# Performance work log

Hardware: AMD Instinct MI355X
Metric: run time of the kernel (lower is better)

The kernel has to match this reference:

```python
import jax, jax.numpy as jnp
import numpy as np

R = 0.2                 # ball-query radius (Descriptor.r)
MAX_NBRS = 64           # CONFIG['Descriptor']['max_num_neighbors']


def setup_inputs() -> dict:
    key = jax.random.key(0)
    k1, k2, k3, k4, k5, k6 = jax.random.split(key, 6)
    N, F, M = 100000, 64, 2048
    x = jax.random.normal(k1, (N, F), dtype=jnp.float32)
    pos = jax.random.normal(k2, (N, 3), dtype=jnp.float32)
    batch = jnp.sort(jax.random.randint(k3, (N,), 0, 4, dtype=jnp.int64))
    key_idx = jax.random.randint(k4, (M,), 0, N, dtype=jnp.int64)
    # MLP params: Linear(F+3 -> 128), ReLU, Linear(128 -> 128)
    H = 128
    W1 = jax.random.normal(k5, (F + 3, H), dtype=jnp.float32) / np.sqrt(F + 3)
    b1 = jnp.zeros((H,), dtype=jnp.float32)
    W2 = jax.random.normal(k6, (H, H), dtype=jnp.float32) / np.sqrt(H)
    b2 = jnp.zeros((H,), dtype=jnp.float32)
    return {"x": x, "pos": pos, "W1": W1, "b1": b1, "W2": W2, "b2": b2,
            "batch": batch, "key_idx": key_idx}


def reference(x, pos, W1, b1, W2, b2, batch, key_idx):
    N = pos.shape[0]
    qpos = pos[key_idx]            # [M,3]
    qbatch = batch[key_idx]        # [M]

    # Brute-force ball query (what torch-cluster radius does under the hood):
    # squared distances via ||q||^2 + ||p||^2 - 2 q.p  -> [M,N]
    d2 = (jnp.sum(qpos * qpos, -1)[:, None]
          + jnp.sum(pos * pos, -1)[None, :]
          - 2.0 * qpos @ pos.T)
    valid = (d2 <= R * R) & (qbatch[:, None] == batch[None, :])   # [M,N]

    # Take the first MAX_NBRS valid neighbors per query (index order, as PyG).
    order_key = jnp.where(valid, jnp.arange(N)[None, :], N)       # invalid -> N
    neg_vals, idx = jax.lax.top_k(-order_key, MAX_NBRS)           # [M,K]
    valid_k = neg_vals > -N                                       # [M,K] real edge mask

    # PointNetConv message: nn(concat([x_j, pos_j - pos_i])), then max-aggregate.
    x_j = x[idx]                                  # [M,K,F] gather
    rel = pos[idx] - qpos[:, None, :]             # [M,K,3]
    h = jnp.concatenate([x_j, rel], axis=-1)      # [M,K,F+3]
    h = jax.nn.relu(h @ W1 + b1)
    h = h @ W2 + b2                               # [M,K,H]
    h = jnp.where(valid_k[..., None], h, -jnp.inf)
    out = jnp.max(h, axis=1)                      # [M,H] max-scatter
    out = jnp.where(jnp.any(valid_k, axis=1)[:, None], out, 0.0)

    # F.normalize(out, dim=-1)
    out = out / jnp.maximum(jnp.linalg.norm(out, axis=-1, keepdims=True), 1e-12)
    return out
```

## Files before the change

### kernel.cpp

```cpp
#include <hip/hip_runtime.h>
#include <math.h>

#define MAXK 64
#define HDIM 128
#define FDIM 64

typedef __attribute__((ext_vector_type(8))) short bf16x8;
typedef __attribute__((ext_vector_type(4))) float f32x4;

__device__ __forceinline__ unsigned short f2bf(float f) {
    unsigned x = __float_as_uint(f);
    unsigned r = (x + 0x7fffu + ((x >> 16) & 1u)) >> 16;
    return (unsigned short)r;
}

__global__ __launch_bounds__(256) void prep_kernel(
    const float* __restrict__ W1, const float* __restrict__ W2,
    unsigned short* __restrict__ W1bf, unsigned short* __restrict__ W2bf)
{
    int t = blockIdx.x * 256 + threadIdx.x;
    if (t < 1536) {
        int s = t;
        int cb = s / 192, rem = s % 192, ks = rem / 64, lane = rem % 64;
        int col = cb*16 + (lane & 15);
        int k0  = ks*32 + (lane >> 4)*8;
        unsigned short v[8];
        #pragma unroll
        for (int j = 0; j < 8; ++j) {
            int k = k0 + j;
            v[j] = (k < 67) ? f2bf(W1[k*HDIM + col]) : (unsigned short)0;
        }
        uint4 p;
        p.x = (unsigned)v[0] | ((unsigned)v[1] << 16);
        p.y = (unsigned)v[2] | ((unsigned)v[3] << 16);
        p.z = (unsigned)v[4] | ((unsigned)v[5] << 16);
        p.w = (unsigned)v[6] | ((unsigned)v[7] << 16);
        *reinterpret_cast<uint4*>(&W1bf[(size_t)s*8]) = p;
    } else if (t < 1536 + 2048) {
        int s = t - 1536;
        int cb = s >> 8, ks = (s >> 6) & 3, lane = s & 63;
        int col = cb*16 + (lane & 15);
        int k0  = ks*32 + (lane >> 4)*8;
        unsigned short v[8];
        #pragma unroll
        for (int j = 0; j < 8; ++j) v[j] = f2bf(W2[(k0+j)*HDIM + col]);
        uint4 p;
        p.x = (unsigned)v[0] | ((unsigned)v[1] << 16);
        p.y = (unsigned)v[2] | ((unsigned)v[3] << 16);
        p.z = (unsigned)v[4] | ((unsigned)v[5] << 16);
        p.w = (unsigned)v[6] | ((unsigned)v[7] << 16);
        *reinterpret_cast<uint4*>(&W2bf[(size_t)s*8]) = p;
    }
}

__global__ __launch_bounds__(64) void scan_kernel(
    const float* __restrict__ pos, const int* __restrict__ batch,
    const int* __restrict__ key_idx, int N,
    int* __restrict__ lists, int* __restrict__ lcnt)
{
    int b = blockIdx.x;
    int m = b >> 2, w = b & 3;
    int lane = threadIdx.x;

    int qi = key_idx[m];
    int qb = batch[qi];
    float qx = pos[3*qi+0], qy = pos[3*qi+1], qz = pos[3*qi+2];

    int lo, hi;
    { int a=0, e=N;  while (a<e){ int mid=(a+e)>>1; if (batch[mid] <  qb) a=mid+1; else e=mid; } lo=a; }
    { int a=lo, e=N; while (a<e){ int mid=(a+e)>>1; if (batch[mid] <= qb) a=mid+1; else e=mid; } hi=a; }

    const float R2 = 0.04f;
    float q2 = __fadd_rn(__fadd_rn(__fmul_rn(qx,qx), __fmul_rn(qy,qy)), __fmul_rn(qz,qz));

    int seg   = hi - lo;
    int qlen  = (seg + 3) >> 2;
    int start = lo + w*qlen;
    int qend  = min(start + qlen, hi);

    int lc = 0;
    for (int base = start; base < qend && lc < MAXK; base += 256) {
        unsigned long long mk[4]; bool vv[4]; int jj[4];
        #pragma unroll
        for (int sub = 0; sub < 4; ++sub) {
            int j = base + sub*64 + lane;
            bool v = false;
            if (j < qend) {
                float px = pos[3*j+0], py = pos[3*j+1], pz = pos[3*j+2];
                float p2 = __fadd_rn(__fadd_rn(__fmul_rn(px,px), __fmul_rn(py,py)), __fmul_rn(pz,pz));
                float dt = __fadd_rn(__fadd_rn(__fmul_rn(qx,px), __fmul_rn(qy,py)), __fmul_rn(qz,pz));
                float d2 = __fsub_rn(__fadd_rn(q2, p2), __fmul_rn(2.0f, dt));
                v = (d2 <= R2);
            }
            mk[sub] = __ballot(v); vv[sub] = v; jj[sub] = j;
        }
        #pragma unroll
        for (int sub = 0; sub < 4; ++sub) {
            if (vv[sub]) {
                int slot = lc + (int)__popcll(mk[sub] & ((1ull << lane) - 1ull));
                if (slot < MAXK) lists[b*MAXK + slot] = jj[sub];
            }
            lc += (int)__popcll(mk[sub]);
        }
    }
    if (lane == 0) lcnt[b] = min(lc, MAXK);
}

__global__ __launch_bounds__(256) void mlp_kernel(
    const float* __restrict__ x, const float* __restrict__ pos,
    const unsigned short* __restrict__ W1bf, const unsigned short* __restrict__ W2bf,
    const float* __restrict__ b1, const float* __restrict__ b2,
    const int* __restrict__ key_idx,
    const int* __restrict__ lists, const int* __restrict__ lcnt,
    float* __restrict__ out, int M)
{
    __shared__ __align__(16) unsigned short a_lds[4*3*64*8];
    __shared__ __align__(16) unsigned short h_lds[4*16*128];
    __shared__ int   nidx[MAXK];
    __shared__ float pmax_s[4][HDIM];
    __shared__ float rsum[2];

    int m   = blockIdx.x;
    int tid = threadIdx.x;
    int lane = tid & 63, w = tid >> 6;
    int colq = lane & 15, rq = lane >> 4;

    int qi = key_idx[m];
    float qx = pos[3*qi+0], qy = pos[3*qi+1], qz = pos[3*qi+2];

    int c0 = lcnt[m*4+0], c1 = lcnt[m*4+1], c2 = lcnt[m*4+2], c3 = lcnt[m*4+3];
    int cnt = min(MAXK, c0 + c1 + c2 + c3);
    if (tid < cnt) {
        int k = tid, q, off;
        if      (k < c0)       { q = 0; off = k; }
        else if (k < c0+c1)    { q = 1; off = k - c0; }
        else if (k < c0+c1+c2) { q = 2; off = k - c0 - c1; }
        else                   { q = 3; off = k - c0 - c1 - c2; }
        nidx[tid] = lists[(m*4+q)*MAXK + off];
    }
    __syncthreads();

    #pragma unroll
    for (int i = 0; i < 3; ++i) {
        int s = tid + i*256;
        int rb = s / 192, rem = s % 192, ks = rem / 64, ln = rem % 64;
        int row = rb*16 + (ln & 15);
        int k0  = ks*32 + (ln >> 4)*8;
        unsigned short v[8];
        #pragma unroll
        for (int j = 0; j < 8; ++j) v[j] = 0;
        if (row < cnt) {
            int idx = nidx[row];
            if (ks < 2) {
                const float4* xp = reinterpret_cast<const float4*>(x + (size_t)idx*FDIM + k0);
                float4 v0 = xp[0], v1 = xp[1];
                v[0]=f2bf(v0.x); v[1]=f2bf(v0.y); v[2]=f2bf(v0.z); v[3]=f2bf(v0.w);
                v[4]=f2bf(v1.x); v[5]=f2bf(v1.y); v[6]=f2bf(v1.z); v[7]=f2bf(v1.w);
            } else if ((ln >> 4) == 0) {
                v[0] = f2bf(pos[3*idx+0] - qx);
                v[1] = f2bf(pos[3*idx+1] - qy);
                v[2] = f2bf(pos[3*idx+2] - qz);
            }
        }
        uint4 p;
        p.x = (unsigned)v[0] | ((unsigned)v[1] << 16);
        p.y = (unsigned)v[2] | ((unsigned)v[3] << 16);
        p.z = (unsigned)v[4] | ((unsigned)v[5] << 16);
        p.w = (unsigned)v[6] | ((unsigned)v[7] << 16);
        *reinterpret_cast<uint4*>(&a_lds[(size_t)s*8]) = p;
    }
    __syncthreads();

    const bf16x8* W1f = reinterpret_cast<const bf16x8*>(W1bf);
    const bf16x8* W2f = reinterpret_cast<const bf16x8*>(W2bf);

    bf16x8 a0 = *reinterpret_cast<const bf16x8*>(&a_lds[((w*3+0)*64 + lane)*8]);
    bf16x8 a1 = *reinterpret_cast<const bf16x8*>(&a_lds[((w*3+1)*64 + lane)*8]);
    bf16x8 a2 = *reinterpret_cast<const bf16x8*>(&a_lds[((w*3+2)*64 + lane)*8]);
    #pragma unroll
    for (int cb = 0; cb < 8; ++cb) {
        f32x4 c = {0.f, 0.f, 0.f, 0.f};
        c = __builtin_amdgcn_mfma_f32_16x16x32_bf16(a0, W1f[(cb*3+0)*64 + lane], c, 0, 0, 0);
        c = __builtin_amdgcn_mfma_f32_16x16x32_bf16(a1, W1f[(cb*3+1)*64 + lane], c, 0, 0, 0);
        c = __builtin_amdgcn_mfma_f32_16x16x32_bf16(a2, W1f[(cb*3+2)*64 + lane], c, 0, 0, 0);
        int col = cb*16 + colq;
        float bias = b1[col];
        #pragma unroll
        for (int reg = 0; reg < 4; ++reg) {
            int r = rq*4 + reg;
            float h = fmaxf(c[reg] + bias, 0.f);
            h_lds[w*2048 + r*128 + (col ^ ((r & 7) << 3))] = f2bf(h);
        }
    }

    int r = colq, swz = (r & 7) << 3;
    bf16x8 g0 = *reinterpret_cast<const bf16x8*>(&h_lds[w*2048 + r*128 + ((  0 + rq*8) ^ swz)]);
    bf16x8 g1 = *reinterpret_cast<const bf16x8*>(&h_lds[w*2048 + r*128 + (( 32 + rq*8) ^ swz)]);
    bf16x8 g2 = *reinterpret_cast<const bf16x8*>(&h_lds[w*2048 + r*128 + (( 64 + rq*8) ^ swz)]);
    bf16x8 g3 = *reinterpret_cast<const bf16x8*>(&h_lds[w*2048 + r*128 + (( 96 + rq*8) ^ swz)]);
    #pragma unroll
    for (int cb = 0; cb < 8; ++cb) {
        f32x4 c = {0.f, 0.f, 0.f, 0.f};
        c = __builtin_amdgcn_mfma_f32_16x16x32_bf16(g0, W2f[(cb*4+0)*64 + lane], c, 0, 0, 0);
        c = __builtin_amdgcn_mfma_f32_16x16x32_bf16(g1, W2f[(cb*4+1)*64 + lane], c, 0, 0, 0);
        c = __builtin_amdgcn_mfma_f32_16x16x32_bf16(g2, W2f[(cb*4+2)*64 + lane], c, 0, 0, 0);
        c = __builtin_amdgcn_mfma_f32_16x16x32_bf16(g3, W2f[(cb*4+3)*64 + lane], c, 0, 0, 0);
        int col = cb*16 + colq;
        float bias = b2[col];
        float mx = -INFINITY;
        #pragma unroll
        for (int reg = 0; reg < 4; ++reg) {
            int row = w*16 + rq*4 + reg;
            float val = c[reg] + bias;
            if (row < cnt) mx = fmaxf(mx, val);
        }
        mx = fmaxf(mx, __shfl_xor(mx, 16, 64));
        mx = fmaxf(mx, __shfl_xor(mx, 32, 64));
        if (rq == 0) pmax_s[w][col] = mx;
    }
    __syncthreads();

    int c = tid & 127, g = tid >> 7;
    float v = fmaxf(fmaxf(pmax_s[0][c], pmax_s[1][c]),
                    fmaxf(pmax_s[2][c], pmax_s[3][c]));
    if (cnt == 0) v = 0.f;
    float s = (g == 0) ? v*v : 0.f;
    #pragma unroll
    for (int o = 32; o > 0; o >>= 1) s += __shfl_xor(s, o, 64);
    if (g == 0 && (tid & 63) == 0) rsum[tid >> 6] = s;
    __syncthreads();
    if (g == 0) {
        float nrm = fmaxf(sqrtf(rsum[0] + rsum[1]), 1e-12f);
        out[(size_t)m*HDIM + c] = v / nrm;
    }
}

extern "C" void kernel_launch(void* const* d_in, const int* in_sizes, int n_in,
                              void* d_out, int out_size, void* d_ws, size_t ws_size,
                              hipStream_t stream)
{
    const float* x       = (const float*)d_in[0];
    const float* pos     = (const float*)d_in[1];
    const float* W1      = (const float*)d_in[2];
    const float* b1      = (const float*)d_in[3];
    const float* W2      = (const float*)d_in[4];
    const float* b2      = (const float*)d_in[5];
    const int*   batch   = (const int*)d_in[6];
    const int*   key_idx = (const int*)d_in[7];

    int N = in_sizes[6];
    int M = in_sizes[7];

    unsigned short* W1bf = (unsigned short*)d_ws;
    unsigned short* W2bf = W1bf + 12288;
    int* lists = (int*)(W2bf + 16384);
    int* lcnt  = lists + (size_t)M * 4 * MAXK;

    prep_kernel<<<14, 256, 0, stream>>>(W1, W2, W1bf, W2bf);
    scan_kernel<<<M*4, 64, 0, stream>>>(pos, batch, key_idx, N, lists, lcnt);
    mlp_kernel<<<M, 256, 0, stream>>>(x, pos, W1bf, W2bf, b1, b2, key_idx,
                                      lists, lcnt, (float*)d_out, M);
}
```

Baseline: 149.9 us.

## Precompute padded float4 positions with norms; load MLP A-fragments directly into registers

The prep kernel now writes a float4 array holding each point's xyz and squared norm. The scan kernel reads it with one vector load per point instead of three scalar loads plus a recompute of the norm. The MLP kernel builds the bf16 A operands for the first GEMM directly in registers from global x and posq, dropping the a_lds staging buffer and one block barrier. The cost is an extra pass over N points and 16 bytes per point of workspace.

```diff
diff --git a/kernel.cpp b/kernel.cpp
--- a/kernel.cpp
+++ b/kernel.cpp
@@ -13,10 +13,15 @@
     unsigned r = (x + 0x7fffu + ((x >> 16) & 1u)) >> 16;
     return (unsigned short)r;
 }
+__device__ __forceinline__ unsigned pk2(float a, float b) {
+    return (unsigned)f2bf(a) | ((unsigned)f2bf(b) << 16);
+}
 
 __global__ __launch_bounds__(256) void prep_kernel(
     const float* __restrict__ W1, const float* __restrict__ W2,
-    unsigned short* __restrict__ W1bf, unsigned short* __restrict__ W2bf)
+    const float* __restrict__ pos, int N,
+    unsigned short* __restrict__ W1bf, unsigned short* __restrict__ W2bf,
+    float4* __restrict__ posq)
 {
     int t = blockIdx.x * 256 + threadIdx.x;
     if (t < 1536) {
@@ -50,11 +55,18 @@
         p.z = (unsigned)v[4] | ((unsigned)v[5] << 16);
         p.w = (unsigned)v[6] | ((unsigned)v[7] << 16);
         *reinterpret_cast<uint4*>(&W2bf[(size_t)s*8]) = p;
+    } else {
+        int i = t - 3584;
+        if (i < N) {
+            float px = pos[3*i+0], py = pos[3*i+1], pz = pos[3*i+2];
+            float p2 = __fadd_rn(__fadd_rn(__fmul_rn(px,px), __fmul_rn(py,py)), __fmul_rn(pz,pz));
+            posq[i] = make_float4(px, py, pz, p2);
+        }
     }
 }
 
 __global__ __launch_bounds__(64) void scan_kernel(
-    const float* __restrict__ pos, const int* __restrict__ batch,
+    const float4* __restrict__ posq, const int* __restrict__ batch,
     const int* __restrict__ key_idx, int N,
     int* __restrict__ lists, int* __restrict__ lcnt)
 {
@@ -64,14 +76,14 @@
 
     int qi = key_idx[m];
     int qb = batch[qi];
-    float qx = pos[3*qi+0], qy = pos[3*qi+1], qz = pos[3*qi+2];
+    float4 q4 = posq[qi];
+    float qx = q4.x, qy = q4.y, qz = q4.z, q2 = q4.w;
 
     int lo, hi;
     { int a=0, e=N;  while (a<e){ int mid=(a+e)>>1; if (batch[mid] <  qb) a=mid+1; else e=mid; } lo=a; }
     { int a=lo, e=N; while (a<e){ int mid=(a+e)>>1; if (batch[mid] <= qb) a=mid+1; else e=mid; } hi=a; }
 
     const float R2 = 0.04f;
-    float q2 = __fadd_rn(__fadd_rn(__fmul_rn(qx,qx), __fmul_rn(qy,qy)), __fmul_rn(qz,qz));
 
     int seg   = hi - lo;
     int qlen  = (seg + 3) >> 2;
@@ -86,10 +98,9 @@
             int j = base + sub*64 + lane;
             bool v = false;
             if (j < qend) {
-                float px = pos[3*j+0], py = pos[3*j+1], pz = pos[3*j+2];
-                float p2 = __fadd_rn(__fadd_rn(__fmul_rn(px,px), __fmul_rn(py,py)), __fmul_rn(pz,pz));
-                float dt = __fadd_rn(__fadd_rn(__fmul_rn(qx,px), __fmul_rn(qy,py)), __fmul_rn(qz,pz));
-                float d2 = __fsub_rn(__fadd_rn(q2, p2), __fmul_rn(2.0f, dt));
+                float4 p = posq[j];
+                float dt = __fadd_rn(__fadd_rn(__fmul_rn(qx,p.x), __fmul_rn(qy,p.y)), __fmul_rn(qz,p.z));
+                float d2 = __fsub_rn(__fadd_rn(q2, p.w), __fmul_rn(2.0f, dt));
                 v = (d2 <= R2);
             }
             mk[sub] = __ballot(v); vv[sub] = v; jj[sub] = j;
@@ -107,14 +118,13 @@
 }
 
 __global__ __launch_bounds__(256) void mlp_kernel(
-    const float* __restrict__ x, const float* __restrict__ pos,
+    const float* __restrict__ x, const float4* __restrict__ posq,
     const unsigned short* __restrict__ W1bf, const unsigned short* __restrict__ W2bf,
     const float* __restrict__ b1, const float* __restrict__ b2,
     const int* __restrict__ key_idx,
     const int* __restrict__ lists, const int* __restrict__ lcnt,
     float* __restrict__ out, int M)
 {
-    __shared__ __align__(16) unsigned short a_lds[4*3*64*8];
     __shared__ __align__(16) unsigned short h_lds[4*16*128];
     __shared__ int   nidx[MAXK];
     __shared__ float pmax_s[4][HDIM];
@@ -126,7 +136,7 @@
     int colq = lane & 15, rq = lane >> 4;
 
     int qi = key_idx[m];
-    float qx = pos[3*qi+0], qy = pos[3*qi+1], qz = pos[3*qi+2];
+    float4 q4 = posq[qi];
 
     int c0 = lcnt[m*4+0], c1 = lcnt[m*4+1], c2 = lcnt[m*4+2], c3 = lcnt[m*4+3];
     int cnt = min(MAXK, c0 + c1 + c2 + c3);
@@ -140,49 +150,35 @@
     }
     __syncthreads();
 
-    #pragma unroll
-    for (int i = 0; i < 3; ++i) {
-        int s = tid + i*256;
-        int rb = s / 192, rem = s % 192, ks = rem / 64, ln = rem % 64;
-        int row = rb*16 + (ln & 15);
-        int k0  = ks*32 + (ln >> 4)*8;
-        unsigned short v[8];
-        #pragma unroll
-        for (int j = 0; j < 8; ++j) v[j] = 0;
-        if (row < cnt) {
-            int idx = nidx[row];
-            if (ks < 2) {
-                const float4* xp = reinterpret_cast<const float4*>(x + (size_t)idx*FDIM + k0);
-                float4 v0 = xp[0], v1 = xp[1];
-                v[0]=f2bf(v0.x); v[1]=f2bf(v0.y); v[2]=f2bf(v0.z); v[3]=f2bf(v0.w);
-                v[4]=f2bf(v1.x); v[5]=f2bf(v1.y); v[6]=f2bf(v1.z); v[7]=f2bf(v1.w);
-            } else if ((ln >> 4) == 0) {
-                v[0] = f2bf(pos[3*idx+0] - qx);
-                v[1] = f2bf(pos[3*idx+1] - qy);
-                v[2] = f2bf(pos[3*idx+2] - qz);
-            }
-        }
-        uint4 p;
-        p.x = (unsigned)v[0] | ((unsigned)v[1] << 16);
-        p.y = (unsigned)v[2] | ((unsigned)v[3] << 16);
-        p.z = (unsigned)v[4] | ((unsigned)v[5] << 16);
-        p.w = (unsigned)v[6] | ((unsigned)v[7] << 16);
-        *reinterpret_cast<uint4*>(&a_lds[(size_t)s*8]) = p;
-    }
-    __syncthreads();
+    int row = w*16 + colq;
+    union { bf16x8 v; uint4 u; } A0, A1, A2;
+    A0.u = make_uint4(0,0,0,0); A1.u = A0.u; A2.u = A0.u;
+    if (row < cnt) {
+        int idx = nidx[row];
+        const float4* xp = reinterpret_cast<const float4*>(x + (size_t)idx*FDIM + rq*8);
+        float4 u0 = xp[0], u1 = xp[1];
+        const float4* xq = reinterpret_cast<const float4*>(x + (size_t)idx*FDIM + 32 + rq*8);
+        float4 u2 = xq[0], u3 = xq[1];
+        A0.u.x = pk2(u0.x, u0.y); A0.u.y = pk2(u0.z, u0.w);
+        A0.u.z = pk2(u1.x, u1.y); A0.u.w = pk2(u1.z, u1.w);
+        A1.u.x = pk2(u2.x, u2.y); A1.u.y = pk2(u2.z, u2.w);
+        A1.u.z = pk2(u3.x, u3.y); A1.u.w = pk2(u3.z, u3.w);
+        if (rq == 0) {
+            float4 p = posq[idx];
+            A2.u.x = pk2(p.x - q4.x, p.y - q4.y);
+            A2.u.y = pk2(p.z - q4.z, 0.f);
+        }
+    }
 
     const bf16x8* W1f = reinterpret_cast<const bf16x8*>(W1bf);
     const bf16x8* W2f = reinterpret_cast<const bf16x8*>(W2bf);
 
-    bf16x8 a0 = *reinterpret_cast<const bf16x8*>(&a_lds[((w*3+0)*64 + lane)*8]);
-    bf16x8 a1 = *reinterpret_cast<const bf16x8*>(&a_lds[((w*3+1)*64 + lane)*8]);
-    bf16x8 a2 = *reinterpret_cast<const bf16x8*>(&a_lds[((w*3+2)*64 + lane)*8]);
     #pragma unroll
     for (int cb = 0; cb < 8; ++cb) {
         f32x4 c = {0.f, 0.f, 0.f, 0.f};
-        c = __builtin_amdgcn_mfma_f32_16x16x32_bf16(a0, W1f[(cb*3+0)*64 + lane], c, 0, 0, 0);
-        c = __builtin_amdgcn_mfma_f32_16x16x32_bf16(a1, W1f[(cb*3+1)*64 + lane], c, 0, 0, 0);
-        c = __builtin_amdgcn_mfma_f32_16x16x32_bf16(a2, W1f[(cb*3+2)*64 + lane], c, 0, 0, 0);
+        c = __builtin_amdgcn_mfma_f32_16x16x32_bf16(A0.v, W1f[(cb*3+0)*64 + lane], c, 0, 0, 0);
+        c = __builtin_amdgcn_mfma_f32_16x16x32_bf16(A1.v, W1f[(cb*3+1)*64 + lane], c, 0, 0, 0);
+        c = __builtin_amdgcn_mfma_f32_16x16x32_bf16(A2.v, W1f[(cb*3+2)*64 + lane], c, 0, 0, 0);
         int col = cb*16 + colq;
         float bias = b1[col];
         #pragma unroll
@@ -210,9 +206,9 @@
         float mx = -INFINITY;
         #pragma unroll
         for (int reg = 0; reg < 4; ++reg) {
-            int row = w*16 + rq*4 + reg;
+            int rr = w*16 + rq*4 + reg;
             float val = c[reg] + bias;
-            if (row < cnt) mx = fmaxf(mx, val);
+            if (rr < cnt) mx = fmaxf(mx, val);
         }
         mx = fmaxf(mx, __shfl_xor(mx, 16, 64));
         mx = fmaxf(mx, __shfl_xor(mx, 32, 64));
@@ -253,11 +249,13 @@
 
     unsigned short* W1bf = (unsigned short*)d_ws;
     unsigned short* W2bf = W1bf + 12288;
-    int* lists = (int*)(W2bf + 16384);
+    float4* posq = (float4*)(W2bf + 16384);
+    int* lists = (int*)(posq + N);
     int* lcnt  = lists + (size_t)M * 4 * MAXK;
 
-    prep_kernel<<<14, 256, 0, stream>>>(W1, W2, W1bf, W2bf);
-    scan_kernel<<<M*4, 64, 0, stream>>>(pos, batch, key_idx, N, lists, lcnt);
-    mlp_kernel<<<M, 256, 0, stream>>>(x, pos, W1bf, W2bf, b1, b2, key_idx,
+    int prep_blocks = (3584 + N + 255) / 256;
+    prep_kernel<<<prep_blocks, 256, 0, stream>>>(W1, W2, pos, N, W1bf, W2bf, posq);
+    scan_kernel<<<M*4, 64, 0, stream>>>(posq, batch, key_idx, N, lists, lcnt);
+    mlp_kernel<<<M, 256, 0, stream>>>(x, posq, W1bf, W2bf, b1, b2, key_idx,
                                       lists, lcnt, (float*)d_out, M);
 }
```

Result: no change. 148.1 us (-1.2%).
